# Optimization experiments

Measured on AMD Instinct MI355X. Metric: run time of the kernel, lower is better.

Reference implementation:

```python
import jax, jax.numpy as jnp
import numpy as np

EMB = 512
HEADS = 8
QKV = 512
WIN = 256  # 'range' init arg, >1 so W = range


def setup_inputs() -> dict:
    key = jax.random.key(0)
    ks = jax.random.split(key, 9)
    B, N = 2, 4096
    s_in = 1.0 / np.sqrt(EMB)
    s_qkv = 1.0 / np.sqrt(QKV)
    return {
        "x": jax.random.normal(ks[0], (B, N, EMB), jnp.float32),
        "Wq": jax.random.normal(ks[1], (EMB, QKV), jnp.float32) * s_in,
        "bq": jnp.zeros((QKV,), jnp.float32),
        "Wk": jax.random.normal(ks[2], (EMB, QKV), jnp.float32) * s_in,
        "bk": jnp.zeros((QKV,), jnp.float32),
        "Wv": jax.random.normal(ks[3], (EMB, QKV), jnp.float32) * s_in,
        "bv": jnp.zeros((QKV,), jnp.float32),
        "Wfc": jax.random.normal(ks[4], (QKV, EMB), jnp.float32) * s_qkv,
        "bfc": jnp.zeros((EMB,), jnp.float32),
    }


def reference(x, Wq, bq, Wk, bk, Wv, bv, Wfc, bfc):
    B, N, E = x.shape
    hd = QKV // HEADS  # head dim = 64
    # window mask: |i-j| <= W//2 -> 0 else -inf
    idx = jnp.arange(N)
    inwin = jnp.abs(idx[None, :] - idx[:, None]) <= (WIN // 2)
    M = jnp.where(inwin, 0.0, -jnp.inf).astype(x.dtype)  # [N,N]

    def split(h):  # [B,N,QKV] -> [B,H,N,hd]
        return h.reshape(B, N, HEADS, hd).transpose(0, 2, 1, 3)

    q = split(x @ Wq + bq)
    k = split(x @ Wk + bk)
    v = split(x @ Wv + bv)

    scale = 1.0 / np.sqrt(hd)
    attn = jnp.einsum("bhnd,bhmd->bhnm", q, k) * scale + M
    attn = jax.nn.softmax(attn, axis=-1)
    o = jnp.einsum("bhnm,bhmd->bhnd", attn, v)  # [B,H,N,hd]
    o = o.transpose(0, 2, 1, 3).reshape(B, N, QKV)
    return o @ Wfc + bfc
```

## Files before the change

kernel.cpp:

```cpp
#include <hip/hip_runtime.h>
#include <math.h>

typedef __bf16 bf16;
typedef __attribute__((ext_vector_type(8))) __bf16 bf16x8;
typedef __attribute__((ext_vector_type(4))) float f32x4;

#define N_SEQ 4096
#define NEGINF -1e30f

__device__ __forceinline__ void gl_lds16(const void* g, void* l) {
    __builtin_amdgcn_global_load_lds(
        (const __attribute__((address_space(1))) void*)g,
        (__attribute__((address_space(3))) void*)l, 16, 0, 0);
}

__device__ __forceinline__ bf16x8 frag64(const bf16* base, int row, int g) {
    return *(const bf16x8*)(base + (row << 6) + ((g ^ (row & 7)) << 3));
}

__global__ __launch_bounds__(256) void cast_x_k(const float* __restrict__ x,
                                                bf16* __restrict__ xb) {
    int idx = blockIdx.x * 256 + threadIdx.x;
    const float4* xv = (const float4*)x;
    float4 a = xv[idx * 2], b = xv[idx * 2 + 1];
    bf16x8 o;
    o[0] = (bf16)a.x; o[1] = (bf16)a.y; o[2] = (bf16)a.z; o[3] = (bf16)a.w;
    o[4] = (bf16)b.x; o[5] = (bf16)b.y; o[6] = (bf16)b.z; o[7] = (bf16)b.w;
    ((bf16x8*)xb)[idx] = o;
}

__global__ __launch_bounds__(256) void prep_w_k(
    const float* __restrict__ Wq, const float* __restrict__ bq,
    const float* __restrict__ Wk, const float* __restrict__ bk,
    const float* __restrict__ Wv, const float* __restrict__ bv,
    const float* __restrict__ Wfc, const float* __restrict__ bfc,
    bf16* __restrict__ Wcat, float* __restrict__ bcat) {
    const int t = threadIdx.x;
    const int k0 = blockIdx.x << 6, n0 = blockIdx.y << 6;
    const int sel = n0 >> 9, nloc = n0 & 511;
    const float* W = (sel == 0) ? Wq : (sel == 1) ? Wk : (sel == 2) ? Wv : Wfc;
    const float* bi = (sel == 0) ? bq : (sel == 1) ? bk : (sel == 2) ? bv : bfc;
    __shared__ bf16 tile[64][65];
#pragma unroll
    for (int i = 0; i < 16; i++) {
        int idx = (i << 8) + t;
        int r = idx >> 6, c = idx & 63;
        tile[r][c] = (bf16)W[(size_t)(k0 + r) * 512 + nloc + c];
    }
    __syncthreads();
#pragma unroll
    for (int i = 0; i < 16; i++) {
        int idx = (i << 8) + t;
        int r = idx >> 6, c = idx & 63;
        Wcat[(size_t)(n0 + r) * 512 + k0 + c] = tile[c][r];
    }
    if (blockIdx.x == 0 && t < 64) bcat[n0 + t] = bi[nloc + t];
}

template <int OUT, int BN>
__global__ __launch_bounds__(256) void gemm_bf16_k(
    const bf16* __restrict__ A, const bf16* __restrict__ Bt,
    const float* __restrict__ bias, void* __restrict__ Cout) {
    constexpr int NI = BN / 32;
    constexpr int BIT = BN / 32;
    __shared__ bf16 sA[2][128 * 64];
    __shared__ bf16 sB[2][BN * 64];
    const int t = threadIdx.x;
    const int lane = t & 63, wid = t >> 6;
    const int wr = wid >> 1, wc = wid & 1;
    const int m0 = blockIdx.x << 7;
    const int n0 = blockIdx.y * BN;

    f32x4 acc[4][NI] = {};

    const bf16* Ag = A + ((size_t)m0 << 9);
    const bf16* Bg = Bt + ((size_t)n0 << 9);

#define STAGE(buf, k0)                                                      \
    {                                                                       \
        _Pragma("unroll") for (int i = 0; i < 4; i++) {                     \
            int gid = (i << 8) + t;                                         \
            int row = gid >> 3, gs = ((gid & 7) ^ (row & 7)) << 3;          \
            gl_lds16(Ag + ((size_t)row << 9) + (k0) + gs, &sA[buf][gid << 3]); \
        }                                                                   \
        _Pragma("unroll") for (int i = 0; i < BIT; i++) {                   \
            int gid = (i << 8) + t;                                         \
            int row = gid >> 3, gs = ((gid & 7) ^ (row & 7)) << 3;          \
            gl_lds16(Bg + ((size_t)row << 9) + (k0) + gs, &sB[buf][gid << 3]); \
        }                                                                   \
    }

    STAGE(0, 0);
    __syncthreads();

    int buf = 0;
    for (int kt = 0; kt < 8; kt++) {
        if (kt < 7) STAGE(buf ^ 1, (kt + 1) << 6);
#pragma unroll
        for (int ks = 0; ks < 2; ks++) {
            int g = (ks << 2) + (lane >> 4);
            bf16x8 af[4], bfr[NI];
#pragma unroll
            for (int mi = 0; mi < 4; mi++)
                af[mi] = frag64(&sA[buf][0], (wr << 6) + (mi << 4) + (lane & 15), g);
#pragma unroll
            for (int ni = 0; ni < NI; ni++)
                bfr[ni] = frag64(&sB[buf][0], wc * (BN / 2) + (ni << 4) + (lane & 15), g);
#pragma unroll
            for (int mi = 0; mi < 4; mi++)
#pragma unroll
                for (int ni = 0; ni < NI; ni++)
                    acc[mi][ni] = __builtin_amdgcn_mfma_f32_16x16x32_bf16(
                        af[mi], bfr[ni], acc[mi][ni], 0, 0, 0);
        }
        __syncthreads();
        buf ^= 1;
    }
#undef STAGE

#pragma unroll
    for (int mi = 0; mi < 4; mi++) {
#pragma unroll
        for (int ni = 0; ni < NI; ni++) {
            int grow0 = m0 + (wr << 6) + (mi << 4) + ((lane >> 4) << 2);
            int gcol = n0 + wc * (BN / 2) + (ni << 4) + (lane & 15);
            float bb = bias[gcol];
#pragma unroll
            for (int r = 0; r < 4; r++) {
                int grow = grow0 + r;
                float v = acc[mi][ni][r] + bb;
                if (OUT == 0) {
                    int b = grow >> 12, n = grow & 4095;
                    int sel = gcol >> 9, rem = gcol & 511;
                    int h = rem >> 6, d = rem & 63;
                    size_t idx =
                        (((size_t)((sel << 4) + (b << 3) + h) * 4096 + n) << 6) + d;
                    ((bf16*)Cout)[idx] = (bf16)v;
                } else {
                    ((float*)Cout)[((size_t)grow << 9) + gcol] = v;
                }
            }
        }
    }
}

__global__ __launch_bounds__(256) void attn_bf16_k(
    const bf16* __restrict__ Q, const bf16* __restrict__ K,
    const bf16* __restrict__ V, bf16* __restrict__ O) {
    __shared__ bf16 QP[8192];
    __shared__ bf16 Ks[2][4096];
    __shared__ bf16 VT[2][4096];

    const int t = threadIdx.x;
    const int lane = t & 63, wid = t >> 6;
    const int bh = blockIdx.x >> 5;
    const int q0 = (blockIdx.x & 31) << 7;

    const bf16* Qp = Q + ((size_t)bh << 18);
    const bf16* Kp = K + ((size_t)bh << 18);
    const bf16* Vp = V + ((size_t)bh << 18);

#pragma unroll
    for (int i = 0; i < 4; i++) {
        int gid = (i << 8) + t;
        int row = gid >> 3, gs = ((gid & 7) ^ (row & 7)) << 3;
        gl_lds16(Qp + ((size_t)(q0 + row) << 6) + gs, &QP[gid << 3]);
    }
    __syncthreads();

    bf16x8 aq[2][2];
#pragma unroll
    for (int b = 0; b < 2; b++)
#pragma unroll
        for (int ks = 0; ks < 2; ks++)
            aq[b][ks] = frag64(QP, (wid << 5) + (b << 4) + (lane & 15),
                               (ks << 2) + (lane >> 4));

    float mrun[2][4], lrun[2][4];
    f32x4 acc_o[2][4] = {};
#pragma unroll
    for (int b = 0; b < 2; b++)
#pragma unroll
        for (int r = 0; r < 4; r++) { mrun[b][r] = NEGINF; lrun[b][r] = 0.f; }

    const int cstart = (q0 >= 128) ? q0 - 128 : 0;
    const int cend = (q0 + 256 <= N_SEQ) ? q0 + 256 : N_SEQ;
    const int nch = (cend - cstart) >> 6;

#define STAGE_KV(c0, sb)                                                     \
    {                                                                        \
        _Pragma("unroll") for (int i = 0; i < 2; i++) {                      \
            int gid = (i << 8) + t;                                          \
            int row = gid >> 3, gs = ((gid & 7) ^ (row & 7)) << 3;           \
            gl_lds16(Kp + ((size_t)((c0) + row) << 6) + gs,                  \
                     &Ks[sb][gid << 3]);                                     \
        }                                                                    \
        int key = t >> 2;                                                    \
        int gd0 = (t & 3) << 1;                                              \
        const uint4* vs = (const uint4*)(Vp + ((size_t)((c0) + key) << 6));  \
        union { uint4 u; bf16 h[8]; } u0, u1;                                \
        u0.u = vs[gd0]; u1.u = vs[gd0 + 1];                                  \
        _Pragma("unroll") for (int e = 0; e < 8; e++) {                      \
            int d0 = (gd0 << 3) + e;                                         \
            VT[sb][(d0 << 6) + (((key >> 3) ^ (d0 & 7)) << 3) + (key & 7)] = \
                u0.h[e];                                                     \
            int d1 = d0 + 8;                                                 \
            VT[sb][(d1 << 6) + (((key >> 3) ^ (d1 & 7)) << 3) + (key & 7)] = \
                u1.h[e];                                                     \
        }                                                                    \
    }

    STAGE_KV(cstart, 0);

    int buf = 0;
    for (int tch = 0; tch < nch; tch++) {
        const int c0 = cstart + (tch << 6);
        __syncthreads();
        if (tch + 1 < nch) STAGE_KV(c0 + 64, buf ^ 1);

        const int rel = c0 - q0;
        const bool masked = (rel != 0) && (rel != 64);

#pragma unroll
        for (int b = 0; b < 2; b++) {
            f32x4 s[4] = {};
#pragma unroll
            for (int ks = 0; ks < 2; ks++) {
                int g = (ks << 2) + (lane >> 4);
#pragma unroll
                for (int ni = 0; ni < 4; ni++) {
                    bf16x8 bk = frag64(&Ks[buf][0], (ni << 4) + (lane & 15), g);
                    s[ni] = __builtin_amdgcn_mfma_f32_16x16x32_bf16(
                        aq[b][ks], bk, s[ni], 0, 0, 0);
                }
            }

            bf16* Pw = &QP[((wid << 1) + b) << 10];
#pragma unroll
            for (int r = 0; r < 4; r++) {
                int rowl = ((lane >> 4) << 2) + r;
                int qi = q0 + (wid << 5) + (b << 4) + rowl;
                float v[4];
                if (masked) {
#pragma unroll
                    for (int ni = 0; ni < 4; ni++) {
                        int kj = c0 + (ni << 4) + (lane & 15);
                        int dd = qi - kj;
                        v[ni] = (dd <= 128 && dd >= -128) ? s[ni][r] * 0.125f
                                                          : NEGINF;
                    }
                } else {
#pragma unroll
                    for (int ni = 0; ni < 4; ni++) v[ni] = s[ni][r] * 0.125f;
                }
                float mx = fmaxf(fmaxf(v[0], v[1]), fmaxf(v[2], v[3]));
#pragma unroll
                for (int off = 1; off < 16; off <<= 1)
                    mx = fmaxf(mx, __shfl_xor(mx, off));
                float mn = fmaxf(mrun[b][r], mx);
                float alpha = __expf(mrun[b][r] - mn);
                float rs = 0.f;
#pragma unroll
                for (int ni = 0; ni < 4; ni++) {
                    float p = __expf(v[ni] - mn);
                    rs += p;
                    int col = (ni << 4) + (lane & 15);
                    Pw[(rowl << 6) + (((col >> 3) ^ (rowl & 7)) << 3) +
                       (col & 7)] = (bf16)p;
                }
#pragma unroll
                for (int off = 1; off < 16; off <<= 1)
                    rs += __shfl_xor(rs, off);
                mrun[b][r] = mn;
                lrun[b][r] = lrun[b][r] * alpha + rs;
#pragma unroll
                for (int nd = 0; nd < 4; nd++) acc_o[b][nd][r] *= alpha;
            }

#pragma unroll
            for (int ks = 0; ks < 2; ks++) {
                int g = (ks << 2) + (lane >> 4);
                bf16x8 pa = frag64(Pw, lane & 15, g);
#pragma unroll
                for (int nd = 0; nd < 4; nd++) {
                    bf16x8 bv = frag64(&VT[buf][0], (nd << 4) + (lane & 15), g);
                    acc_o[b][nd] = __builtin_amdgcn_mfma_f32_16x16x32_bf16(
                        pa, bv, acc_o[b][nd], 0, 0, 0);
                }
            }
        }
        buf ^= 1;
    }
#undef STAGE_KV

    const int bb = bh >> 3, h = bh & 7;
#pragma unroll
    for (int b = 0; b < 2; b++) {
#pragma unroll
        for (int r = 0; r < 4; r++) {
            float inv = 1.f / lrun[b][r];
            int n = q0 + (wid << 5) + (b << 4) + ((lane >> 4) << 2) + r;
#pragma unroll
            for (int nd = 0; nd < 4; nd++) {
                int d = (nd << 4) + (lane & 15);
                O[(((size_t)(bb * 4096 + n)) << 9) + (h << 6) + d] =
                    (bf16)(acc_o[b][nd][r] * inv);
            }
        }
    }
}

extern "C" void kernel_launch(void* const* d_in, const int* in_sizes, int n_in,
                              void* d_out, int out_size, void* d_ws, size_t ws_size,
                              hipStream_t stream) {
    (void)in_sizes; (void)n_in; (void)out_size; (void)ws_size;
    const float* x   = (const float*)d_in[0];
    const float* Wq  = (const float*)d_in[1];
    const float* bq  = (const float*)d_in[2];
    const float* Wk  = (const float*)d_in[3];
    const float* bk  = (const float*)d_in[4];
    const float* Wv  = (const float*)d_in[5];
    const float* bv  = (const float*)d_in[6];
    const float* Wfc = (const float*)d_in[7];
    const float* bfc = (const float*)d_in[8];

    bf16* xb    = (bf16*)d_ws;
    bf16* Wcat  = xb + (size_t)8192 * 512;
    float* bcat = (float*)(Wcat + (size_t)2048 * 512);
    bf16* QKVb  = (bf16*)(bcat + 2048);
    bf16* Ob    = QKVb + (size_t)3 * 16 * 4096 * 64;

    cast_x_k<<<(8192 * 512) / (256 * 8), 256, 0, stream>>>(x, xb);
    prep_w_k<<<dim3(8, 32), 256, 0, stream>>>(Wq, bq, Wk, bk, Wv, bv, Wfc, bfc,
                                              Wcat, bcat);

    gemm_bf16_k<0, 128><<<dim3(64, 12), 256, 0, stream>>>(xb, Wcat, bcat, QKVb);

    const bf16* Qb = QKVb;
    const bf16* Kb = QKVb + ((size_t)1 << 22);
    const bf16* Vb = QKVb + ((size_t)2 << 22);
    attn_bf16_k<<<512, 256, 0, stream>>>(Qb, Kb, Vb, Ob);

    gemm_bf16_k<1, 64><<<dim3(64, 8), 256, 0, stream>>>(
        Ob, Wcat + ((size_t)1536 << 9), bcat + 1536, d_out);
}
```

Measured before the change: 155.0 us.

## Fuse prep kernels, remap blocks per XCD, stage GEMM epilogue through LDS

Merges the x cast and weight transpose into one launch. Remaps GEMM and attention block indices so consecutive tiles land on the same XCD, which should improve L2 locality. Drops GEMM double buffering to a single LDS buffer with an occupancy hint of 3, and rewrites the epilogue to stage results in swizzled LDS and issue 16-byte coalesced global stores instead of scalar scattered stores. The single buffer gives up overlap of loads with MFMA work, betting on higher occupancy to hide that latency instead.

```diff
diff --git a/kernel.cpp b/kernel.cpp
--- a/kernel.cpp
+++ b/kernel.cpp
@@ -18,29 +18,31 @@
     return *(const bf16x8*)(base + (row << 6) + ((g ^ (row & 7)) << 3));
 }
 
-__global__ __launch_bounds__(256) void cast_x_k(const float* __restrict__ x,
-                                                bf16* __restrict__ xb) {
-    int idx = blockIdx.x * 256 + threadIdx.x;
-    const float4* xv = (const float4*)x;
-    float4 a = xv[idx * 2], b = xv[idx * 2 + 1];
-    bf16x8 o;
-    o[0] = (bf16)a.x; o[1] = (bf16)a.y; o[2] = (bf16)a.z; o[3] = (bf16)a.w;
-    o[4] = (bf16)b.x; o[5] = (bf16)b.y; o[6] = (bf16)b.z; o[7] = (bf16)b.w;
-    ((bf16x8*)xb)[idx] = o;
-}
-
-__global__ __launch_bounds__(256) void prep_w_k(
+__global__ __launch_bounds__(256) void prep_k(
+    const float* __restrict__ x, bf16* __restrict__ xb,
     const float* __restrict__ Wq, const float* __restrict__ bq,
     const float* __restrict__ Wk, const float* __restrict__ bk,
     const float* __restrict__ Wv, const float* __restrict__ bv,
     const float* __restrict__ Wfc, const float* __restrict__ bfc,
     bf16* __restrict__ Wcat, float* __restrict__ bcat) {
+    __shared__ bf16 tile[64][65];
     const int t = threadIdx.x;
-    const int k0 = blockIdx.x << 6, n0 = blockIdx.y << 6;
+    const int bx = blockIdx.x;
+    if (bx < 2048) {
+        int idx = bx * 256 + t;
+        const float4* xv = (const float4*)x;
+        float4 a = xv[idx * 2], b = xv[idx * 2 + 1];
+        bf16x8 o;
+        o[0] = (bf16)a.x; o[1] = (bf16)a.y; o[2] = (bf16)a.z; o[3] = (bf16)a.w;
+        o[4] = (bf16)b.x; o[5] = (bf16)b.y; o[6] = (bf16)b.z; o[7] = (bf16)b.w;
+        ((bf16x8*)xb)[idx] = o;
+        return;
+    }
+    const int bz = bx - 2048;
+    const int k0 = (bz & 7) << 6, n0 = (bz >> 3) << 6;
     const int sel = n0 >> 9, nloc = n0 & 511;
     const float* W = (sel == 0) ? Wq : (sel == 1) ? Wk : (sel == 2) ? Wv : Wfc;
     const float* bi = (sel == 0) ? bq : (sel == 1) ? bk : (sel == 2) ? bv : bfc;
-    __shared__ bf16 tile[64][65];
 #pragma unroll
     for (int i = 0; i < 16; i++) {
         int idx = (i << 8) + t;
@@ -54,58 +56,55 @@
         int r = idx >> 6, c = idx & 63;
         Wcat[(size_t)(n0 + r) * 512 + k0 + c] = tile[c][r];
     }
-    if (blockIdx.x == 0 && t < 64) bcat[n0 + t] = bi[nloc + t];
-}
-
-template <int OUT, int BN>
-__global__ __launch_bounds__(256) void gemm_bf16_k(
+    if ((bz & 7) == 0 && t < 64) bcat[n0 + t] = bi[nloc + t];
+}
+
+template <int OUT, int BN, int NT>
+__global__ __launch_bounds__(256, 3) void gemm_bf16_k(
     const bf16* __restrict__ A, const bf16* __restrict__ Bt,
     const float* __restrict__ bias, void* __restrict__ Cout) {
     constexpr int NI = BN / 32;
-    constexpr int BIT = BN / 32;
-    __shared__ bf16 sA[2][128 * 64];
-    __shared__ bf16 sB[2][BN * 64];
+    __shared__ __align__(16) bf16 smem[16384];
+    bf16* sA = smem;
+    bf16* sB = smem + 8192;
     const int t = threadIdx.x;
     const int lane = t & 63, wid = t >> 6;
     const int wr = wid >> 1, wc = wid & 1;
-    const int m0 = blockIdx.x << 7;
-    const int n0 = blockIdx.y * BN;
+    const int wg = blockIdx.x;
+    const int s = (wg & 7) * (8 * NT) + (wg >> 3);
+    const int m_idx = s / NT, n_idx = s - m_idx * NT;
+    const int m0 = m_idx << 7, n0 = n_idx * BN;
 
     f32x4 acc[4][NI] = {};
 
     const bf16* Ag = A + ((size_t)m0 << 9);
     const bf16* Bg = Bt + ((size_t)n0 << 9);
 
-#define STAGE(buf, k0)                                                      \
-    {                                                                       \
-        _Pragma("unroll") for (int i = 0; i < 4; i++) {                     \
-            int gid = (i << 8) + t;                                         \
-            int row = gid >> 3, gs = ((gid & 7) ^ (row & 7)) << 3;          \
-            gl_lds16(Ag + ((size_t)row << 9) + (k0) + gs, &sA[buf][gid << 3]); \
-        }                                                                   \
-        _Pragma("unroll") for (int i = 0; i < BIT; i++) {                   \
-            int gid = (i << 8) + t;                                         \
-            int row = gid >> 3, gs = ((gid & 7) ^ (row & 7)) << 3;          \
-            gl_lds16(Bg + ((size_t)row << 9) + (k0) + gs, &sB[buf][gid << 3]); \
-        }                                                                   \
-    }
-
-    STAGE(0, 0);
-    __syncthreads();
-
-    int buf = 0;
     for (int kt = 0; kt < 8; kt++) {
-        if (kt < 7) STAGE(buf ^ 1, (kt + 1) << 6);
+        const int k0 = kt << 6;
+#pragma unroll
+        for (int i = 0; i < 4; i++) {
+            int gid = (i << 8) + t;
+            int row = gid >> 3, gs = ((gid & 7) ^ (row & 7)) << 3;
+            gl_lds16(Ag + ((size_t)row << 9) + k0 + gs, &sA[gid << 3]);
+        }
+#pragma unroll
+        for (int i = 0; i < NI; i++) {
+            int gid = (i << 8) + t;
+            int row = gid >> 3, gs = ((gid & 7) ^ (row & 7)) << 3;
+            gl_lds16(Bg + ((size_t)row << 9) + k0 + gs, &sB[gid << 3]);
+        }
+        __syncthreads();
 #pragma unroll
         for (int ks = 0; ks < 2; ks++) {
             int g = (ks << 2) + (lane >> 4);
             bf16x8 af[4], bfr[NI];
 #pragma unroll
             for (int mi = 0; mi < 4; mi++)
-                af[mi] = frag64(&sA[buf][0], (wr << 6) + (mi << 4) + (lane & 15), g);
+                af[mi] = frag64(sA, (wr << 6) + (mi << 4) + (lane & 15), g);
 #pragma unroll
             for (int ni = 0; ni < NI; ni++)
-                bfr[ni] = frag64(&sB[buf][0], wc * (BN / 2) + (ni << 4) + (lane & 15), g);
+                bfr[ni] = frag64(sB, wc * (BN / 2) + (ni << 4) + (lane & 15), g);
 #pragma unroll
             for (int mi = 0; mi < 4; mi++)
 #pragma unroll
@@ -114,32 +113,65 @@
                         af[mi], bfr[ni], acc[mi][ni], 0, 0, 0);
         }
         __syncthreads();
-        buf ^= 1;
-    }
-#undef STAGE
-
-#pragma unroll
-    for (int mi = 0; mi < 4; mi++) {
-#pragma unroll
-        for (int ni = 0; ni < NI; ni++) {
-            int grow0 = m0 + (wr << 6) + (mi << 4) + ((lane >> 4) << 2);
-            int gcol = n0 + wc * (BN / 2) + (ni << 4) + (lane & 15);
-            float bb = bias[gcol];
-#pragma unroll
-            for (int r = 0; r < 4; r++) {
-                int grow = grow0 + r;
-                float v = acc[mi][ni][r] + bb;
-                if (OUT == 0) {
-                    int b = grow >> 12, n = grow & 4095;
-                    int sel = gcol >> 9, rem = gcol & 511;
-                    int h = rem >> 6, d = rem & 63;
-                    size_t idx =
-                        (((size_t)((sel << 4) + (b << 3) + h) * 4096 + n) << 6) + d;
-                    ((bf16*)Cout)[idx] = (bf16)v;
-                } else {
-                    ((float*)Cout)[((size_t)grow << 9) + gcol] = v;
-                }
-            }
+    }
+
+    float bb[NI];
+#pragma unroll
+    for (int ni = 0; ni < NI; ni++)
+        bb[ni] = bias[n0 + wc * (BN / 2) + (ni << 4) + (lane & 15)];
+
+    if (OUT == 0) {
+        bf16* cs = smem;
+#pragma unroll
+        for (int mi = 0; mi < 4; mi++)
+#pragma unroll
+            for (int ni = 0; ni < NI; ni++)
+#pragma unroll
+                for (int r = 0; r < 4; r++) {
+                    int row = (wr << 6) + (mi << 4) + ((lane >> 4) << 2) + r;
+                    int col = (wc << 6) + (ni << 4) + (lane & 15);
+                    int g = col >> 3;
+                    cs[(row << 7) + ((g ^ (row & 7)) << 3) + (col & 7)] =
+                        (bf16)(acc[mi][ni][r] + bb[ni]);
+                }
+        __syncthreads();
+        int row = t >> 1, half = t & 1;
+        int gm = m0 + row;
+        int b = gm >> 12, n = gm & 4095;
+#pragma unroll
+        for (int j = 0; j < 8; j++) {
+            int g = (half << 3) + j;
+            bf16x8 v = *(bf16x8*)&cs[(row << 7) + ((g ^ (row & 7)) << 3)];
+            int gc = n0 + (g << 3);
+            int sel = gc >> 9, rem = gc & 511;
+            int h = rem >> 6, d = rem & 63;
+            *(bf16x8*)&(
+                ((bf16*)Cout)[(((size_t)((sel << 4) + (b << 3) + h) * 4096 + n)
+                               << 6) +
+                              d]) = v;
+        }
+    } else {
+        float* cs = (float*)smem;
+#pragma unroll
+        for (int mi = 0; mi < 4; mi++)
+#pragma unroll
+            for (int ni = 0; ni < NI; ni++)
+#pragma unroll
+                for (int r = 0; r < 4; r++) {
+                    int row = (wr << 6) + (mi << 4) + ((lane >> 4) << 2) + r;
+                    int col = (wc << 5) + (ni << 4) + (lane & 15);
+                    int g4 = col >> 2;
+                    cs[(row << 6) + ((g4 ^ (row & 7)) << 2) + (col & 3)] =
+                        acc[mi][ni][r] + bb[ni];
+                }
+        __syncthreads();
+        int row = t >> 1, half = t & 1;
+#pragma unroll
+        for (int j = 0; j < 8; j++) {
+            int g4 = (half << 3) + j;
+            f32x4 v = *(f32x4*)&cs[(row << 6) + ((g4 ^ (row & 7)) << 2)];
+            *(f32x4*)&(
+                ((float*)Cout)[(size_t)(m0 + row) * 512 + n0 + (g4 << 2)]) = v;
         }
     }
 }
@@ -153,8 +185,10 @@
 
     const int t = threadIdx.x;
     const int lane = t & 63, wid = t >> 6;
-    const int bh = blockIdx.x >> 5;
-    const int q0 = (blockIdx.x & 31) << 7;
+    const int wg = blockIdx.x;
+    const int sblk = ((wg & 7) << 6) + (wg >> 3);
+    const int bh = sblk >> 5;
+    const int q0 = (sblk & 31) << 7;
 
     const bf16* Qp = Q + ((size_t)bh << 18);
     const bf16* Kp = K + ((size_t)bh << 18);
@@ -330,17 +364,16 @@
     bf16* QKVb  = (bf16*)(bcat + 2048);
     bf16* Ob    = QKVb + (size_t)3 * 16 * 4096 * 64;
 
-    cast_x_k<<<(8192 * 512) / (256 * 8), 256, 0, stream>>>(x, xb);
-    prep_w_k<<<dim3(8, 32), 256, 0, stream>>>(Wq, bq, Wk, bk, Wv, bv, Wfc, bfc,
-                                              Wcat, bcat);
-
-    gemm_bf16_k<0, 128><<<dim3(64, 12), 256, 0, stream>>>(xb, Wcat, bcat, QKVb);
+    prep_k<<<2304, 256, 0, stream>>>(x, xb, Wq, bq, Wk, bk, Wv, bv, Wfc, bfc,
+                                     Wcat, bcat);
+
+    gemm_bf16_k<0, 128, 12><<<768, 256, 0, stream>>>(xb, Wcat, bcat, QKVb);
 
     const bf16* Qb = QKVb;
     const bf16* Kb = QKVb + ((size_t)1 << 22);
     const bf16* Vb = QKVb + ((size_t)2 << 22);
     attn_bf16_k<<<512, 256, 0, stream>>>(Qb, Kb, Vb, Ob);
 
-    gemm_bf16_k<1, 64><<<dim3(64, 8), 256, 0, stream>>>(
+    gemm_bf16_k<1, 64, 8><<<512, 256, 0, stream>>>(
         Ob, Wcat + ((size_t)1536 << 9), bcat + 1536, d_out);
 }
```

Result: no change. 153.7 us (-0.8%).
